# Kernel tuning notes

Measured on AMD Instinct MI355X. Metric: run time of the kernel, lower is better.

Reference implementation:

```python
import jax, jax.numpy as jnp
import numpy as np

B, T = 64, 20
VOCAB, E, CE, ANS = 20000, 300, 1024, 3000
H, N, W, R = 512, 256, 64, 4
RW = R * W
IF_SIZES = [RW, R, W, 1, W, W, R, 1, 1, 3 * R]  # read_keys, read_str, write_key, write_str, erase, write_vec, free, alloc_g, write_g, modes
IF_TOT = sum(IF_SIZES)
CLIP = 20.0
EPS = 1e-6


def _cosine_weights(mem, keys, strengths):
    # mem [B,N,W], keys [B,K,W], strengths [B,K] -> softmax over N
    mem_n = mem / (jnp.linalg.norm(mem, axis=-1, keepdims=True) + EPS)
    key_n = keys / (jnp.linalg.norm(keys, axis=-1, keepdims=True) + EPS)
    sim = jnp.einsum('bkw,bnw->bkn', key_n, mem_n)
    return jax.nn.softmax(sim * strengths[..., None], axis=-1)


def _init_state(b):
    z = lambda *s: jnp.zeros(s, jnp.float32)
    return (z(b, N, W), z(b, N, N), z(b, N), z(b, R, N), z(b, N), z(b, N), z(b, R, W), z(b, H), z(b, H))


def _dnc_step(Wih, Whh, b, Wif, bif, Wout, bout, state, x):
    mem, link, prec, wr, ww, usage, rvec, h, c = state
    bsz = x.shape[0]
    inp = jnp.concatenate([x, rvec.reshape(bsz, RW)], -1)
    gates = inp @ Wih + h @ Whh + b
    gi, gf, gg, go = jnp.split(gates, 4, -1)
    c = jax.nn.sigmoid(gf) * c + jax.nn.sigmoid(gi) * jnp.tanh(gg)
    h = jax.nn.sigmoid(go) * jnp.tanh(c)
    hc = jnp.clip(h, -CLIP, CLIP)
    xi = hc @ Wif + bif
    p = jnp.split(xi, np.cumsum(IF_SIZES)[:-1].tolist(), axis=-1)
    read_keys = jnp.tanh(p[0]).reshape(bsz, R, W)
    read_str = jax.nn.softplus(p[1])
    write_key = jnp.tanh(p[2]).reshape(bsz, 1, W)
    write_str = jax.nn.softplus(p[3])
    erase = jax.nn.sigmoid(p[4])
    write_vec = jnp.tanh(p[5])
    free = jax.nn.sigmoid(p[6])
    alloc_g = jax.nn.sigmoid(p[7])
    write_g = jax.nn.sigmoid(p[8])
    modes = jax.nn.softmax(p[9].reshape(bsz, R, 3), -1)

    # usage update and allocation (sort-based, data dependent)
    psi = jnp.prod(1.0 - free[..., None] * wr, axis=1)          # [B,N]
    usage = (usage + ww - usage * ww) * psi
    s_idx = jnp.argsort(usage, axis=-1)                          # ascending usage
    s_u = jnp.take_along_axis(usage, s_idx, -1)
    cp = jnp.cumprod(jnp.concatenate([jnp.ones_like(s_u[:, :1]), s_u[:, :-1]], -1), -1)
    a_sorted = (1.0 - s_u) * cp
    inv = jnp.argsort(s_idx, axis=-1)
    alloc = jnp.take_along_axis(a_sorted, inv, -1)

    # write
    cw = _cosine_weights(mem, write_key, write_str)[:, 0]        # [B,N]
    ww = write_g * (alloc_g * alloc + (1.0 - alloc_g) * cw)
    mem = mem * (1.0 - ww[..., None] * erase[:, None, :]) + ww[..., None] * write_vec[:, None, :]

    # temporal link matrix
    link = (1.0 - ww[:, :, None] - ww[:, None, :]) * link + ww[:, :, None] * prec[:, None, :]
    link = link * (1.0 - jnp.eye(N, dtype=link.dtype))
    prec = (1.0 - ww.sum(-1, keepdims=True)) * prec + ww

    # read
    fw = jnp.einsum('bij,brj->bri', link, wr)
    bw = jnp.einsum('bji,brj->bri', link, wr)
    cr = _cosine_weights(mem, read_keys, read_str)
    wr = modes[..., 0:1] * bw + modes[..., 1:2] * cr + modes[..., 2:3] * fw
    rvec = jnp.einsum('brn,bnw->brw', wr, mem)

    out = jnp.concatenate([hc, rvec.reshape(bsz, RW)], -1) @ Wout + bout
    out = jnp.clip(out, -CLIP, CLIP)
    return (mem, link, prec, wr, ww, usage, rvec, h, c), out


def _model(img_feat, emb, img_W, img_b, q_Wih, q_Whh, q_b, q_Wif, q_bif, q_Wout, q_bout,
           c_Wih, c_Whh, c_b, c_Wif, c_bif, c_Wout, c_bout, fc1_W, fc1_b, fc2_W, fc2_b, qst):
    bsz = qst.shape[0]
    # question encoder: embedding -> tanh -> DNC over time -> mean pool
    qv = jnp.tanh(emb[qst])                                      # [B,T,E]
    step = lambda st, x: _dnc_step(q_Wih, q_Whh, q_b, q_Wif, q_bif, q_Wout, q_bout, st, x)
    _, outs = jax.lax.scan(step, _init_state(bsz), jnp.swapaxes(qv, 0, 1))
    qfeat = outs.mean(0)                                         # [B,CE]
    # image encoder: fc on frozen VGG feature, L2 norm (norm detached)
    imgf = img_feat @ img_W + img_b
    imgf = imgf / jax.lax.stop_gradient(jnp.linalg.norm(imgf, axis=1, keepdims=True))
    comb = jnp.tanh(imgf * qfeat)
    # controller DNC: single timestep
    st_c, out_c = _dnc_step(c_Wih, c_Whh, c_b, c_Wif, c_bif, c_Wout, c_bout, _init_state(bsz), comb)
    rv_c = st_c[6].reshape(bsz, RW)
    last = jnp.tanh(jnp.concatenate([out_c, rv_c], -1))
    last = jnp.tanh(last @ fc1_W + fc1_b)
    return last @ fc2_W + fc2_b                                  # logits [B,ANS]


def setup_inputs():
    ks = jax.random.split(jax.random.key(0), 20)
    g = lambda k, s, sc=0.05: jax.random.normal(k, s, dtype=jnp.float32) * sc
    z = lambda *s: jnp.zeros(s, jnp.float32)
    return {
        'img_feat': g(ks[0], (B, 4096), 1.0),
        'qst': jax.random.randint(ks[1], (B, T), 0, VOCAB),
        'emb': g(ks[2], (VOCAB, E)),
        'img_W': g(ks[3], (4096, CE)), 'img_b': z(CE),
        'q_Wih': g(ks[4], (E + RW, 4 * H)), 'q_Whh': g(ks[5], (H, 4 * H)), 'q_b': z(4 * H),
        'q_Wif': g(ks[6], (H, IF_TOT)), 'q_bif': z(IF_TOT),
        'q_Wout': g(ks[7], (H + RW, CE)), 'q_bout': z(CE),
        'c_Wih': g(ks[8], (CE + RW, 4 * H)), 'c_Whh': g(ks[9], (H, 4 * H)), 'c_b': z(4 * H),
        'c_Wif': g(ks[10], (H, IF_TOT)), 'c_bif': z(IF_TOT),
        'c_Wout': g(ks[11], (H + RW, CE)), 'c_bout': z(CE),
        'fc1_W': g(ks[12], (CE + RW, ANS)), 'fc1_b': z(ANS),
        'fc2_W': g(ks[13], (ANS, ANS)), 'fc2_b': z(ANS),
    }


def reference(img_feat, qst, emb, img_W, img_b, q_Wih, q_Whh, q_b, q_Wif, q_bif, q_Wout, q_bout,
              c_Wih, c_Whh, c_b, c_Wif, c_bif, c_Wout, c_bout, fc1_W, fc1_b, fc2_W, fc2_b):
    return _model(img_feat, emb, img_W, img_b, q_Wih, q_Whh, q_b, q_Wif, q_bif, q_Wout, q_bout,
                  c_Wih, c_Whh, c_b, c_Wif, c_bif, c_Wout, c_bout, fc1_W, fc1_b, fc2_W, fc2_b, qst)
```

## Files before the change

### kernel.cpp

```cpp
#include <hip/hip_runtime.h>
#include <cmath>

#define CLIPV 20.0f
#define EPSV 1e-6f

__device__ __forceinline__ float sigmoidf_(float x){ return 1.0f/(1.0f + expf(-x)); }
__device__ __forceinline__ float softplusf_(float x){ return (x > 20.0f) ? x : log1pf(expf(x)); }
__device__ __forceinline__ float clipf_(float x){ return fminf(fmaxf(x, -CLIPV), CLIPV); }

__device__ __forceinline__ float wave_sum64(float v){
  #pragma unroll
  for (int off=32; off>=1; off>>=1) v += __shfl_xor(v, off, 64);
  return v;
}
__device__ __forceinline__ float wave_max64(float v){
  #pragma unroll
  for (int off=32; off>=1; off>>=1) v = fmaxf(v, __shfl_xor(v, off, 64));
  return v;
}
__device__ __forceinline__ float block_sum256(float v, float* s_red){
  v = wave_sum64(v);
  __syncthreads();
  if ((threadIdx.x & 63) == 0) s_red[threadIdx.x>>6] = v;
  __syncthreads();
  return s_red[0]+s_red[1]+s_red[2]+s_red[3];
}
__device__ __forceinline__ float block_max256(float v, float* s_red){
  v = wave_max64(v);
  __syncthreads();
  if ((threadIdx.x & 63) == 0) s_red[threadIdx.x>>6] = v;
  __syncthreads();
  return fmaxf(fmaxf(s_red[0],s_red[1]), fmaxf(s_red[2],s_red[3]));
}
template<int N>
__device__ __forceinline__ void block_sumN(float (&v)[N], float* scr){
  #pragma unroll
  for (int i=0;i<N;i++) v[i] = wave_sum64(v[i]);
  __syncthreads();
  if ((threadIdx.x & 63) == 0){
    int w = threadIdx.x >> 6;
    #pragma unroll
    for (int i=0;i<N;i++) scr[w*N + i] = v[i];
  }
  __syncthreads();
  #pragma unroll
  for (int i=0;i<N;i++) v[i] = scr[0*N+i] + scr[1*N+i] + scr[2*N+i] + scr[3*N+i];
}
template<int N>
__device__ __forceinline__ void block_maxN(float (&v)[N], float* scr){
  #pragma unroll
  for (int i=0;i<N;i++) v[i] = wave_max64(v[i]);
  __syncthreads();
  if ((threadIdx.x & 63) == 0){
    int w = threadIdx.x >> 6;
    #pragma unroll
    for (int i=0;i<N;i++) scr[w*N + i] = v[i];
  }
  __syncthreads();
  #pragma unroll
  for (int i=0;i<N;i++) v[i] = fmaxf(fmaxf(scr[0*N+i],scr[1*N+i]), fmaxf(scr[2*N+i],scr[3*N+i]));
}

__device__ __forceinline__ void cstore(float* p, float v){
  __hip_atomic_store(p, v, __ATOMIC_RELAXED, __HIP_MEMORY_SCOPE_AGENT);
}

#define WS_MEM    0
#define WS_LINK   1048576
#define WS_PREC   5242880
#define WS_WR     5275648
#define WS_WW     5341184
#define WS_USAGE  5357568
#define WS_BAR    5373952
#define WS_ZONEA  5374976
#define WS_QSUM   5374976
#define WS_HTS    5440512
#define WS_RVS    6128640
#define WS_XIS    6472704
#define WS_GXP    7105728
#define WS_ZONEC  9727168
#define WS_IMGF   10879168
#define WS_COMB   10944704
#define WS_LASTB  11010240
#define WS_HID1   11092160
#define WS_QV     11284160

__global__ void embed_kernel(const int* __restrict__ qst, const float* __restrict__ emb,
                             float* __restrict__ qv){
  int idx = blockIdx.x*256 + threadIdx.x;
  if (idx >= 1280*300) return;
  int m = idx / 300;
  int e = idx - m*300;
  int t = m >> 6, b = m & 63;
  int tok = qst[b*20 + t];
  qv[idx] = tanhf(emb[(size_t)tok*300 + e]);
}

__global__ __launch_bounds__(256) void gemm64(
    int M, int N, int Ktot, int KS,
    const float* __restrict__ A, int lda,
    const float* __restrict__ B,
    const float* __restrict__ bias,
    float* __restrict__ out, float* __restrict__ part, int mode)
{
  __shared__ float As[32*68];
  __shared__ float Bs[32*68];
  int tid = threadIdx.x;
  int nb = blockIdx.x*64, ks = blockIdx.y, mb = blockIdx.z*64;
  int Kc = (((Ktot + KS - 1)/KS) + 3) & ~3;
  int kbeg = ks*Kc, kend = min(Ktot, kbeg + Kc);
  int tm = tid >> 4, tn = tid & 15;
  float acc[4][4];
  #pragma unroll
  for (int i=0;i<4;i++){ acc[i][0]=0.f; acc[i][1]=0.f; acc[i][2]=0.f; acc[i][3]=0.f; }

  for (int k0 = kbeg; k0 < kend; k0 += 32){
    int klim = kend - k0; if (klim > 32) klim = 32;
    #pragma unroll
    for (int i=0;i<2;i++){
      int idx = tid + i*256;
      int m = idx >> 3, kq = (idx & 7) << 2;
      if (kq < klim){
        const float* ap = A + (size_t)(mb+m)*lda + k0 + kq;
        float4 v;
        if (kq + 3 < klim) v = *(const float4*)ap;
        else { v.x=ap[0]; v.y=(kq+1<klim)?ap[1]:0.f; v.z=(kq+2<klim)?ap[2]:0.f; v.w=0.f; }
        float* as = As + m;
        as[(kq+0)*68]=v.x; as[(kq+1)*68]=v.y; as[(kq+2)*68]=v.z; as[(kq+3)*68]=v.w;
      }
    }
    #pragma unroll
    for (int i=0;i<2;i++){
      int idx = tid + i*256;
      int kk = idx >> 4, nq = (idx & 15) << 2;
      int n = nb + nq;
      float4 v = {0.f,0.f,0.f,0.f};
      if (kk < klim && n < N){
        const float* bp = B + (size_t)(k0+kk)*N + n;
        if (n + 3 < N) v = *(const float4*)bp;
        else { v.x=bp[0]; v.y=(n+1<N)?bp[1]:0.f; v.z=(n+2<N)?bp[2]:0.f; }
      }
      *(float4*)(Bs + kk*68 + nq) = v;
    }
    __syncthreads();
    for (int kk = 0; kk < klim; kk++){
      float4 a = *(const float4*)(As + kk*68 + tm*4);
      float4 bv = *(const float4*)(Bs + kk*68 + tn*4);
      acc[0][0]+=a.x*bv.x; acc[0][1]+=a.x*bv.y; acc[0][2]+=a.x*bv.z; acc[0][3]+=a.x*bv.w;
      acc[1][0]+=a.y*bv.x; acc[1][1]+=a.y*bv.y; acc[1][2]+=a.y*bv.z; acc[1][3]+=a.y*bv.w;
      acc[2][0]+=a.z*bv.x; acc[2][1]+=a.z*bv.y; acc[2][2]+=a.z*bv.z; acc[2][3]+=a.z*bv.w;
      acc[3][0]+=a.w*bv.x; acc[3][1]+=a.w*bv.y; acc[3][2]+=a.w*bv.z; acc[3][3]+=a.w*bv.w;
    }
    __syncthreads();
  }

  #pragma unroll
  for (int i=0;i<4;i++){
    int m = tm*4 + i;
    #pragma unroll
    for (int j=0;j<4;j++){
      int n = nb + tn*4 + j;
      if (n < N){
        if (mode == 0){
          part[((size_t)(ks*64 + m))*N + n] = acc[i][j];
        } else {
          float v = acc[i][j] + (bias ? bias[n] : 0.f);
          if (mode == 2) v = tanhf(v);
          out[(size_t)(mb+m)*N + n] = v;
        }
      }
    }
  }
}

__global__ void reduce64(const float* __restrict__ part, int KS, int MN4, int N,
                         const float* __restrict__ bias, float* __restrict__ out, int mode){
  int idx = blockIdx.x*256 + threadIdx.x;
  if (idx >= MN4) return;
  int base = idx*4;
  int n = base % N;
  float4 s = {0.f,0.f,0.f,0.f};
  size_t stride = (size_t)MN4*4;
  for (int p=0;p<KS;p++){
    float4 t = *(const float4*)(part + (size_t)p*stride + base);
    s.x+=t.x; s.y+=t.y; s.z+=t.z; s.w+=t.w;
  }
  if (bias){
    float4 bb = *(const float4*)(bias + n);
    s.x+=bb.x; s.y+=bb.y; s.z+=bb.z; s.w+=bb.w;
  }
  if (mode == 1){ s.x=tanhf(s.x); s.y=tanhf(s.y); s.z=tanhf(s.z); s.w=tanhf(s.w); }
  *(float4*)(out + base) = s;
}

__global__ __launch_bounds__(256) void comb_kernel(const float* __restrict__ imgf,
                                                   const float* __restrict__ qsum,
                                                   float* __restrict__ comb){
  __shared__ float s_red[4];
  int b = blockIdx.x, tid = threadIdx.x;
  float ss = 0.f;
  for (int j = tid; j < 1024; j += 256){ float v = imgf[b*1024+j]; ss += v*v; }
  ss = wave_sum64(ss);
  if ((tid & 63) == 0) s_red[tid>>6] = ss;
  __syncthreads();
  float inv = 1.0f / sqrtf(s_red[0]+s_red[1]+s_red[2]+s_red[3]);
  for (int j = tid; j < 1024; j += 256)
    comb[b*1024+j] = tanhf(imgf[b*1024+j]*inv * qsum[b*1024+j]*0.05f);
}

__global__ void tanhrvec_kernel(const float* __restrict__ rvecT, float* __restrict__ lastB){
  int idx = blockIdx.x*256 + threadIdx.x;
  if (idx >= 16384) return;
  int b = idx & 63, i = idx >> 6;
  lastB[(size_t)b*1280 + 1024 + i] = tanhf(rvecT[i*64 + b]);
}

struct SD_t {
  float s_rk[256], s_rstr[4], s_wkey[64], s_erase[64], s_wvec[64];
  float s_free[4], s_modes[12], s_scal[3], s_pad0[1];
  float s_wr[1024];
  float s_wwnew[256], s_usage[256], s_prec[256], s_scan[256], s_sim[256];
  float s_C[1024], s_D[1024];
  float s_red[44], s_PQ[8];
};
struct SGLO_t { float red[4*768]; float g2[768]; };
struct Shm {
  float Wg[768*8];
  float Wo[768*4];
  float Wi[512*4];
  union { SGLO_t glo; SD_t d; } u;
};


__device__ __forceinline__ void gbar(int* subs, int* root, int* ggen, int epoch){
  __syncthreads();
  if (threadIdx.x == 0){
    asm volatile("s_waitcnt vmcnt(0)" ::: "memory");
    int g = blockIdx.x & 15;
    int old = __hip_atomic_fetch_add(&subs[g*16], 1, __ATOMIC_RELAXED, __HIP_MEMORY_SCOPE_AGENT);
    if (old == 16*epoch - 1){
      int r = __hip_atomic_fetch_add(root, 1, __ATOMIC_RELAXED, __HIP_MEMORY_SCOPE_AGENT);
      if (r == 16*epoch - 1){
        #pragma unroll
        for (int gg = 0; gg < 16; gg++)
          __hip_atomic_store(&ggen[gg*16], epoch, __ATOMIC_RELAXED, __HIP_MEMORY_SCOPE_AGENT);
      }
    }
    while (__hip_atomic_load(&ggen[g*16], __ATOMIC_RELAXED, __HIP_MEMORY_SCOPE_AGENT) < epoch)
      __builtin_amdgcn_s_sleep(2);
    asm volatile("" ::: "memory");
  }
  __syncthreads();
}

__global__ __launch_bounds__(256) void dnc_recur(
    int T, int outmode, int slot0,
    const float* __restrict__ xpart, const float* __restrict__ Wih_r,
    const float* __restrict__ Whh, const float* __restrict__ gb,
    const float* __restrict__ Wif, const float* __restrict__ bif,
    const float* __restrict__ Wout, const float* __restrict__ bout,
    float* __restrict__ ws, float* __restrict__ outbuf, int* __restrict__ barmem)
{
  __shared__ Shm sh;

  float* memS  = ws + WS_MEM;
  float* linkS = ws + WS_LINK;
  float* precB = ws + WS_PREC;
  float* wrS   = ws + WS_WR;
  float* wwS   = ws + WS_WW;
  float* usgS  = ws + WS_USAGE;
  float* htS   = ws + WS_HTS;
  float* rvS   = ws + WS_RVS;
  float* xiSl  = ws + WS_XIS;
  int* subs  = barmem;
  int* root  = barmem + 256;
  int* ggen  = barmem + 288;
  int* xict  = barmem + 576;
  int* subsH = barmem + 608;
  int* rootH = barmem + 896;

  int tid = threadIdx.x, bid = blockIdx.x;
  int lane = tid & 63, wid = tid >> 6;
  int b_ = tid & 63, q_ = tid >> 6;

  {
    int c2 = bid*2;
    float2* Wg2w = (float2*)sh.Wg;
    for (int e2 = tid; e2 < 3072; e2 += 256){
      int k = e2 >> 2, g = e2 & 3;
      const float* src = (k < 256) ? (Wih_r + (size_t)k*2048 + g*512 + c2)
                                   : (Whh + (size_t)(k-256)*2048 + g*512 + c2);
      Wg2w[e2] = *(const float2*)src;
    }
    int c4o = bid*4;
    float4* Wo4 = (float4*)sh.Wo;
    for (int k = tid; k < 768; k += 256)
      Wo4[k] = *(const float4*)(Wout + (size_t)k*1024 + c4o);
    if (bid < 118){
      for (int e = tid; e < 2048; e += 256){
        int k = e >> 2, c = e & 3;
        int col = c4o + c;
        sh.Wi[e] = (col < 471) ? Wif[(size_t)k*471 + col] : 0.f;
      }
    }
  }
  float bo = bout[bid*4 + q_];
  float bifv = 0.f;
  if (bid < 118 && bid*4 + q_ < 471) bifv = bif[bid*4 + q_];
  __syncthreads();

  float c_reg = 0.f;
  float qacc = 0.f;

  for (int t = 0; t < T; t++){
    int pp = t & 1, wp = (t + 1) & 1;

    {
      if (t > 0){
        float accG[8] = {0.f,0.f,0.f,0.f,0.f,0.f,0.f,0.f};
        float accO[4] = {0.f,0.f,0.f,0.f};
        const float* rvP = rvS + (size_t)(slot0+t-1)*16384;
        const float* hP  = htS + (size_t)(slot0+t-1)*32768;
        for (int c = 0; c < 12; c++){
          int k0 = c*64 + wid*16;
          bool isH = (k0 >= 256);
          const float* src = isH ? (hP + (size_t)(k0-256)*64) : (rvP + (size_t)k0*64);
          float a[16];
          #pragma unroll
          for (int u=0; u<16; u++) a[u] = src[u*64 + lane];
          #pragma unroll
          for (int u=0; u<16; u++){
            int k = k0 + u;
            float4 w0 = *(const float4*)(sh.Wg + (size_t)k*8);
            float4 w1 = *(const float4*)(sh.Wg + (size_t)k*8 + 4);
            int orow = isH ? (k - 256) : (512 + k);
            float4 wo = *(const float4*)(sh.Wo + (size_t)orow*4);
            float av = a[u];
            float ao = isH ? clipf_(av) : av;
            accG[0] += av*w0.x; accG[1] += av*w0.y; accG[2] += av*w0.z; accG[3] += av*w0.w;
            accG[4] += av*w1.x; accG[5] += av*w1.y; accG[6] += av*w1.z; accG[7] += av*w1.w;
            accO[0] += ao*wo.x; accO[1] += ao*wo.y; accO[2] += ao*wo.z; accO[3] += ao*wo.w;
          }
        }
        #pragma unroll
        for (int j=0;j<8;j++) sh.u.glo.red[wid*768 + j*64 + lane] = accG[j];
        #pragma unroll
        for (int j=0;j<4;j++) sh.u.glo.red[wid*768 + (8+j)*64 + lane] = accO[j];
      }
      __syncthreads();
      #pragma unroll
      for (int v=0; v<3; v++){
        int j = q_ + v*4;
        float s;
        if (j < 8){
          int col = (j>>1)*512 + bid*2 + (j&1);
          s = gb[col] + xpart[((size_t)(t*64 + b_))*2048 + col];
        } else {
          s = bo;
        }
        if (t > 0){
          s += sh.u.glo.red[0*768 + j*64 + b_];
          s += sh.u.glo.red[1*768 + j*64 + b_];
          s += sh.u.glo.red[2*768 + j*64 + b_];
          s += sh.u.glo.red[3*768 + j*64 + b_];
        }
        sh.u.glo.g2[j*64 + b_] = s;
      }
      __syncthreads();
      if (t > 0) qacc += clipf_(sh.u.glo.g2[(8+q_)*64 + b_]);
      if (tid < 128){
        int jj = q_;
        float gi = sh.u.glo.g2[(0+jj)*64 + b_];
        float gf = sh.u.glo.g2[(2+jj)*64 + b_];
        float gg = sh.u.glo.g2[(4+jj)*64 + b_];
        float go = sh.u.glo.g2[(6+jj)*64 + b_];
        float cn = sigmoidf_(gf)*c_reg + sigmoidf_(gi)*tanhf(gg);
        float hn = sigmoidf_(go)*tanhf(cn);
        c_reg = cn;
        int col = bid*2 + jj;
        cstore(&htS[(size_t)(slot0+t)*32768 + col*64 + b_], hn);
      }
    }

    __syncthreads();
    if (tid == 0){
      asm volatile("s_waitcnt vmcnt(0)" ::: "memory");
      int g = bid & 15;
      int old = __hip_atomic_fetch_add(&subsH[g*16], 1, __ATOMIC_RELAXED, __HIP_MEMORY_SCOPE_AGENT);
      if (old == 16*(t+1) - 1)
        __hip_atomic_fetch_add(rootH, 1, __ATOMIC_RELAXED, __HIP_MEMORY_SCOPE_AGENT);
    }

    if (bid < 118){
      if (tid == 0){
        while (__hip_atomic_load(rootH, __ATOMIC_RELAXED, __HIP_MEMORY_SCOPE_AGENT) < 16*(t+1))
          __builtin_amdgcn_s_sleep(1);
        asm volatile("" ::: "memory");
      }
      __syncthreads();
      float acc[4] = {0.f,0.f,0.f,0.f};
      const float* hP = htS + (size_t)(slot0+t)*32768;
      for (int c = 0; c < 8; c++){
        int k0 = c*64 + wid*16;
        float a[16];
        #pragma unroll
        for (int u=0; u<16; u++) a[u] = hP[(size_t)(k0+u)*64 + lane];
        #pragma unroll
        for (int u=0; u<16; u++){
          float4 wv = *(const float4*)(sh.Wi + (size_t)(k0+u)*4);
          float ac = clipf_(a[u]);
          acc[0] += ac*wv.x; acc[1] += ac*wv.y; acc[2] += ac*wv.z; acc[3] += ac*wv.w;
        }
      }
      #pragma unroll
      for (int j=0;j<4;j++) sh.u.glo.red[wid*256 + j*64 + lane] = acc[j];
      __syncthreads();
      {
        float s = bifv;
        #pragma unroll
        for (int w=0;w<4;w++) s += sh.u.glo.red[w*256 + q_*64 + b_];
        int col = bid*4 + q_;
        if (col < 471) cstore(&xiSl[(size_t)(slot0+t)*30144 + b_*471 + col], s);
      }
      __syncthreads();
      if (tid == 0)
        __hip_atomic_fetch_add(xict, 1, __ATOMIC_RELAXED, __HIP_MEMORY_SCOPE_AGENT);
    }

    if (bid < 64){
      SD_t& sd = sh.u.d;
      int b = bid;
      const float* prec_in  = precB + pp*16384;
      float*       prec_out = precB + wp*16384;

      for (int e = tid; e < 1024; e += 256){
        sd.s_wr[e] = wrS[(size_t)b*1024 + e];
        sd.s_C[e] = 0.f; sd.s_D[e] = 0.f;
      }
      float wwold = wwS[(size_t)b*256 + tid];
      sd.s_usage[tid] = usgS[(size_t)b*256 + tid];
      sd.s_prec[tid]  = prec_in[(size_t)b*256 + tid];

      if (tid == 0){
        while (__hip_atomic_load(xict, __ATOMIC_RELAXED, __HIP_MEMORY_SCOPE_AGENT) < 118*(t+1))
          __builtin_amdgcn_s_sleep(1);
        asm volatile("" ::: "memory");
      }
      __syncthreads();

      const float* xrow = xiSl + (size_t)(slot0+t)*30144 + (size_t)b*471;
      for (int idx = tid; idx < 471; idx += 256){
        float v = xrow[idx];
        if (idx < 256)       sd.s_rk[idx] = tanhf(v);
        else if (idx < 260)  sd.s_rstr[idx-256] = softplusf_(v);
        else if (idx < 324)  sd.s_wkey[idx-260] = v;
        else if (idx == 324) sd.s_scal[0] = softplusf_(v);
        else if (idx < 389)  sd.s_erase[idx-325] = sigmoidf_(v);
        else if (idx < 453)  sd.s_wvec[idx-389] = tanhf(v);
        else if (idx < 457)  sd.s_free[idx-453] = sigmoidf_(v);
        else if (idx == 457) sd.s_scal[1] = sigmoidf_(v);
        else if (idx == 458) sd.s_scal[2] = sigmoidf_(v);
        else                 sd.s_modes[idx-459] = v;
      }
      __syncthreads();

      if (tid < 4){
        float m0 = sd.s_modes[tid*3], m1 = sd.s_modes[tid*3+1], m2 = sd.s_modes[tid*3+2];
        float mx = fmaxf(m0, fmaxf(m1,m2));
        float e0 = expf(m0-mx), e1 = expf(m1-mx), e2 = expf(m2-mx);
        float s = e0+e1+e2;
        sd.s_modes[tid*3] = e0/s; sd.s_modes[tid*3+1] = e1/s; sd.s_modes[tid*3+2] = e2/s;
      }
      {
        float k = sd.s_rk[wid*64 + lane];
        float ss = wave_sum64(k*k);
        sd.s_rk[wid*64 + lane] = k / (sqrtf(ss) + EPSV);
      }
      if (wid == 0){
        float k = sd.s_wkey[lane];
        float ss = wave_sum64(k*k);
        sd.s_wkey[lane] = k / (sqrtf(ss) + EPSV);
      }

      {
        float psi = 1.f;
        #pragma unroll
        for (int r=0;r<4;r++) psi *= (1.f - sd.s_free[r]*sd.s_wr[r*256+tid]);
        float u = (sd.s_usage[tid] + wwold - sd.s_usage[tid]*wwold) * psi;
        sd.s_usage[tid] = u;
        usgS[(size_t)b*256 + tid] = u;
      }
      __syncthreads();

      int rank_r;
      {
        float u = sd.s_usage[tid];
        int rank = 0;
        #pragma unroll 4
        for (int j4=0;j4<256;j4+=4){
          float4 uv = *(const float4*)(sd.s_usage + j4);
          rank += (uv.x < u) || (uv.x == u && (j4+0) < tid);
          rank += (uv.y < u) || (uv.y == u && (j4+1) < tid);
          rank += (uv.z < u) || (uv.z == u && (j4+2) < tid);
          rank += (uv.w < u) || (uv.w == u && (j4+3) < tid);
        }
        rank_r = rank;
        sd.s_scan[rank] = u;
      }
      __syncthreads();

      {
        float v = sd.s_scan[tid];
        #pragma unroll
        for (int off=1; off<64; off<<=1){
          float u2 = __shfl_up(v, off, 64);
          if (lane >= off) v *= u2;
        }
        if (lane == 63) sd.s_red[wid] = v;
        __syncthreads();
        float pre = 1.f;
        if (wid > 0) pre *= sd.s_red[0];
        if (wid > 1) pre *= sd.s_red[1];
        if (wid > 2) pre *= sd.s_red[2];
        v *= pre;
        sd.s_scan[tid] = v;
        __syncthreads();
      }
      float alloc_r;
      {
        float u = sd.s_usage[tid];
        float cpe = (rank_r > 0) ? sd.s_scan[rank_r-1] : 1.f;
        alloc_r = (1.f - u) * cpe;
      }

      {
        const float4* Mrow = (const float4*)(memS + (size_t)b*16384 + (size_t)tid*64);
        float nrm2 = 0.f, dt = 0.f;
        #pragma unroll
        for (int c4 = 0; c4 < 16; c4++){
          float4 mv = Mrow[c4];
          int w0 = c4*4;
          nrm2 += mv.x*mv.x + mv.y*mv.y + mv.z*mv.z + mv.w*mv.w;
          dt += mv.x*sd.s_wkey[w0] + mv.y*sd.s_wkey[w0+1] + mv.z*sd.s_wkey[w0+2] + mv.w*sd.s_wkey[w0+3];
        }
        sd.s_sim[tid] = dt / (sqrtf(nrm2)+EPSV) * sd.s_scal[0];
      }
      __syncthreads();

      {
        float v = sd.s_sim[tid];
        float mx = block_max256(v, sd.s_red);
        float e = expf(v - mx);
        float sm = block_sum256(e, sd.s_red);
        float cw = e / sm;
        float wwn = sd.s_scal[2] * (sd.s_scal[1]*alloc_r + (1.f - sd.s_scal[1])*cw);
        sd.s_wwnew[tid] = wwn;
        wwS[(size_t)b*256 + tid] = wwn;
        float r9[9];
        r9[0] = wwn;
        #pragma unroll
        for (int r=0;r<4;r++) r9[1+r] = sd.s_prec[tid]*sd.s_wr[r*256+tid];
        #pragma unroll
        for (int r=0;r<4;r++) r9[5+r] = wwn*sd.s_wr[r*256+tid];
        block_sumN<9>(r9, sd.s_red + 4);
        prec_out[(size_t)b*256 + tid] = (1.f - r9[0])*sd.s_prec[tid] + wwn;
        if (tid == 0){
          #pragma unroll
          for (int r=0;r<4;r++){ sd.s_PQ[r] = r9[1+r]; sd.s_PQ[4+r] = r9[5+r]; }
        }
      }
      __syncthreads();

      float aA[4] = {0,0,0,0}, aB[4] = {0,0,0,0};
      {
        const float4* Lrow = (const float4*)(linkS + (size_t)b*65536 + (size_t)tid*256);
        for (int c4 = 0; c4 < 64; c4++){
          float4 lv = Lrow[c4];
          int j = c4*4;
          float w0n = sd.s_wwnew[j], w1n = sd.s_wwnew[j+1], w2n = sd.s_wwnew[j+2], w3n = sd.s_wwnew[j+3];
          #pragma unroll
          for (int r=0;r<4;r++){
            float wr0 = sd.s_wr[r*256+j], wr1 = sd.s_wr[r*256+j+1];
            float wr2 = sd.s_wr[r*256+j+2], wr3 = sd.s_wr[r*256+j+3];
            aA[r] += lv.x*wr0 + lv.y*wr1 + lv.z*wr2 + lv.w*wr3;
            aB[r] += lv.x*(w0n*wr0) + lv.y*(w1n*wr1) + lv.z*(w2n*wr2) + lv.w*(w3n*wr3);
          }
        }
      }
      __syncthreads();

      {
        int cg = tid & 63, ioff = tid >> 6;
        int j0 = cg*4;
        float wwj0 = sd.s_wwnew[j0], wwj1 = sd.s_wwnew[j0+1], wwj2 = sd.s_wwnew[j0+2], wwj3 = sd.s_wwnew[j0+3];
        float pj0 = sd.s_prec[j0], pj1 = sd.s_prec[j0+1], pj2 = sd.s_prec[j0+2], pj3 = sd.s_prec[j0+3];
        float cC[4][4] = {{0}}, cD[4][4] = {{0}};
        float4* Lb = (float4*)(linkS + (size_t)b*65536);
        for (int it = 0; it < 64; it++){
          int i = it*4 + ioff;
          float4 lv = Lb[(size_t)i*64 + cg];
          float wwi = sd.s_wwnew[i];
          float4 ln;
          ln.x = (1.f - wwi - wwj0)*lv.x + wwi*pj0;
          ln.y = (1.f - wwi - wwj1)*lv.y + wwi*pj1;
          ln.z = (1.f - wwi - wwj2)*lv.z + wwi*pj2;
          ln.w = (1.f - wwi - wwj3)*lv.w + wwi*pj3;
          if (i >= j0 && i < j0+4){
            if (i == j0)        ln.x = 0.f;
            else if (i == j0+1) ln.y = 0.f;
            else if (i == j0+2) ln.z = 0.f;
            else                ln.w = 0.f;
          }
          Lb[(size_t)i*64 + cg] = ln;
          #pragma unroll
          for (int r=0;r<4;r++){
            float wri = sd.s_wr[r*256+i];
            float vbi = wwi*wri;
            cC[r][0] += lv.x*wri; cC[r][1] += lv.y*wri; cC[r][2] += lv.z*wri; cC[r][3] += lv.w*wri;
            cD[r][0] += lv.x*vbi; cD[r][1] += lv.y*vbi; cD[r][2] += lv.z*vbi; cD[r][3] += lv.w*vbi;
          }
        }
        for (int w=0; w<4; w++){
          if (ioff == w){
            #pragma unroll
            for (int r=0;r<4;r++){
              sd.s_C[r*256+j0+0] += cC[r][0]; sd.s_C[r*256+j0+1] += cC[r][1];
              sd.s_C[r*256+j0+2] += cC[r][2]; sd.s_C[r*256+j0+3] += cC[r][3];
              sd.s_D[r*256+j0+0] += cD[r][0]; sd.s_D[r*256+j0+1] += cD[r][1];
              sd.s_D[r*256+j0+2] += cD[r][2]; sd.s_D[r*256+j0+3] += cD[r][3];
            }
          }
          __syncthreads();
        }
      }

      float pr[4];
      {
        float4* Mrow = (float4*)(memS + (size_t)b*16384 + (size_t)tid*64);
        float wwn = sd.s_wwnew[tid];
        float nrm2 = 0.f, d0=0.f, d1=0.f, d2=0.f, d3=0.f;
        #pragma unroll
        for (int c4 = 0; c4 < 16; c4++){
          float4 mv = Mrow[c4];
          int w0 = c4*4;
          mv.x = mv.x*(1.f - wwn*sd.s_erase[w0+0]) + wwn*sd.s_wvec[w0+0];
          mv.y = mv.y*(1.f - wwn*sd.s_erase[w0+1]) + wwn*sd.s_wvec[w0+1];
          mv.z = mv.z*(1.f - wwn*sd.s_erase[w0+2]) + wwn*sd.s_wvec[w0+2];
          mv.w = mv.w*(1.f - wwn*sd.s_erase[w0+3]) + wwn*sd.s_wvec[w0+3];
          Mrow[c4] = mv;
          nrm2 += mv.x*mv.x + mv.y*mv.y + mv.z*mv.z + mv.w*mv.w;
          d0 += mv.x*sd.s_rk[w0] + mv.y*sd.s_rk[w0+1] + mv.z*sd.s_rk[w0+2] + mv.w*sd.s_rk[w0+3];
          d1 += mv.x*sd.s_rk[64+w0] + mv.y*sd.s_rk[64+w0+1] + mv.z*sd.s_rk[64+w0+2] + mv.w*sd.s_rk[64+w0+3];
          d2 += mv.x*sd.s_rk[128+w0] + mv.y*sd.s_rk[128+w0+1] + mv.z*sd.s_rk[128+w0+2] + mv.w*sd.s_rk[128+w0+3];
          d3 += mv.x*sd.s_rk[192+w0] + mv.y*sd.s_rk[192+w0+1] + mv.z*sd.s_rk[192+w0+2] + mv.w*sd.s_rk[192+w0+3];
        }
        float inv = 1.f/(sqrtf(nrm2)+EPSV);
        pr[0] = d0*inv*sd.s_rstr[0];
        pr[1] = d1*inv*sd.s_rstr[1];
        pr[2] = d2*inv*sd.s_rstr[2];
        pr[3] = d3*inv*sd.s_rstr[3];
      }
      {
        float m4[4] = {pr[0], pr[1], pr[2], pr[3]};
        block_maxN<4>(m4, sd.s_red + 4);
        float e4[4];
        #pragma unroll
        for (int r=0;r<4;r++) e4[r] = expf(pr[r] - m4[r]);
        float s4[4] = {e4[0], e4[1], e4[2], e4[3]};
        block_sumN<4>(s4, sd.s_red + 4);
        #pragma unroll
        for (int r=0;r<4;r++) pr[r] = e4[r]/s4[r];
      }
      __syncthreads();

      {
        float wwn = sd.s_wwnew[tid], pn = sd.s_prec[tid];
        #pragma unroll
        for (int r=0;r<4;r++){
          float wro = sd.s_wr[r*256+tid];
          float fw  = (1.f-wwn)*aA[r] - aB[r] + wwn*(sd.s_PQ[r] - pn*wro);
          float bwv = (1.f-wwn)*sd.s_C[r*256+tid] - sd.s_D[r*256+tid] + pn*(sd.s_PQ[4+r] - wwn*wro);
          float wrn = sd.s_modes[r*3+0]*bwv + sd.s_modes[r*3+1]*pr[r] + sd.s_modes[r*3+2]*fw;
          wrS[(size_t)b*1024 + r*256 + tid] = wrn;
          sd.s_wr[r*256+tid] = wrn;
        }
      }
      __syncthreads();

      {
        int r = tid >> 6, w = tid & 63;
        const float* Mb = memS + (size_t)b*16384;
        float acc = 0.f;
        for (int n=0; n<256; n++) acc += sd.s_wr[r*256+n]*Mb[(size_t)n*64 + w];
        cstore(&rvS[(size_t)(slot0+t)*16384 + (r*64 + w)*64 + b], acc);
      }
    }

    gbar(subs, root, ggen, t+1);
  }

  {
    float accO[4] = {0.f,0.f,0.f,0.f};
    const float* rvP = rvS + (size_t)(slot0+T-1)*16384;
    const float* hP  = htS + (size_t)(slot0+T-1)*32768;
    for (int c = 0; c < 12; c++){
      int k0 = c*64 + wid*16;
      bool isH = (k0 >= 256);
      const float* src = isH ? (hP + (size_t)(k0-256)*64) : (rvP + (size_t)k0*64);
      float a[16];
      #pragma unroll
      for (int u=0; u<16; u++) a[u] = src[u*64 + lane];
      #pragma unroll
      for (int u=0; u<16; u++){
        int k = k0 + u;
        int orow = isH ? (k - 256) : (512 + k);
        float4 wo = *(const float4*)(sh.Wo + (size_t)orow*4);
        float av = isH ? clipf_(a[u]) : a[u];
        accO[0] += av*wo.x; accO[1] += av*wo.y; accO[2] += av*wo.z; accO[3] += av*wo.w;
      }
    }
    #pragma unroll
    for (int j=0;j<4;j++) sh.u.glo.red[wid*256 + j*64 + lane] = accO[j];
    __syncthreads();
    float v = bo;
    #pragma unroll
    for (int w=0;w<4;w++) v += sh.u.glo.red[w*256 + q_*64 + b_];
    v = clipf_(v);
    if (outmode == 0){
      qacc += v;
      outbuf[(size_t)b_*1024 + (bid*4 + q_)] = qacc;
    } else {
      outbuf[(size_t)b_*1280 + (bid*4 + q_)] = tanhf(v);
    }
  }
}

extern "C" void kernel_launch(void* const* d_in, const int* in_sizes, int n_in,
                              void* d_out, int out_size, void* d_ws, size_t ws_size,
                              hipStream_t stream) {
  const float* img_feat = (const float*)d_in[0];
  const int*   qst      = (const int*)  d_in[1];
  const float* emb      = (const float*)d_in[2];
  const float* img_W    = (const float*)d_in[3];
  const float* img_b    = (const float*)d_in[4];
  const float* q_Wih    = (const float*)d_in[5];
  const float* q_Whh    = (const float*)d_in[6];
  const float* q_b      = (const float*)d_in[7];
  const float* q_Wif    = (const float*)d_in[8];
  const float* q_bif    = (const float*)d_in[9];
  const float* q_Wout   = (const float*)d_in[10];
  const float* q_bout   = (const float*)d_in[11];
  const float* c_Wih    = (const float*)d_in[12];
  const float* c_Whh    = (const float*)d_in[13];
  const float* c_b      = (const float*)d_in[14];
  const float* c_Wif    = (const float*)d_in[15];
  const float* c_bif    = (const float*)d_in[16];
  const float* c_Wout   = (const float*)d_in[17];
  const float* c_bout   = (const float*)d_in[18];
  const float* fc1_W    = (const float*)d_in[19];
  const float* fc1_b    = (const float*)d_in[20];
  const float* fc2_W    = (const float*)d_in[21];
  const float* fc2_b    = (const float*)d_in[22];

  float* ws = (float*)d_ws;
  float* qv    = ws + WS_QV;
  float* gxp   = ws + WS_GXP;
  float* zoneC = ws + WS_ZONEC;
  float* imgf  = ws + WS_IMGF;
  float* combB = ws + WS_COMB;
  float* lastB = ws + WS_LASTB;
  float* hid1  = ws + WS_HID1;
  float* qsum  = ws + WS_QSUM;
  int*   bar   = (int*)(ws + WS_BAR);

  hipMemsetAsync(ws, 0, (size_t)WS_ZONEA*4, stream);

  embed_kernel<<<1500, 256, 0, stream>>>(qst, emb, qv);

  gemm64<<<dim3(16,16,1), 256, 0, stream>>>(64, 1024, 4096, 16,
      img_feat, 4096, img_W, nullptr, nullptr, zoneC, 0);
  reduce64<<<64, 256, 0, stream>>>(zoneC, 16, 16384, 1024, img_b, imgf, 0);

  gemm64<<<dim3(32,1,20), 256, 0, stream>>>(1280, 2048, 300, 1,
      qv, 300, q_Wih, nullptr, gxp, nullptr, 1);

  dnc_recur<<<256, 256, 0, stream>>>(20, 0, 0,
      gxp, q_Wih + (size_t)300*2048, q_Whh, q_b,
      q_Wif, q_bif, q_Wout, q_bout, ws, qsum, bar);

  comb_kernel<<<64, 256, 0, stream>>>(imgf, qsum, combB);

  hipMemsetAsync(ws, 0, (size_t)WS_ZONEA*4, stream);

  gemm64<<<dim3(32,4,1), 256, 0, stream>>>(64, 2048, 1024, 4,
      combB, 1024, c_Wih, nullptr, nullptr, zoneC, 0);
  reduce64<<<128, 256, 0, stream>>>(zoneC, 4, 32768, 2048, nullptr, gxp, 0);

  dnc_recur<<<256, 256, 0, stream>>>(1, 1, 20,
      gxp, c_Wih + (size_t)1024*2048, c_Whh, c_b,
      c_Wif, c_bif, c_Wout, c_bout, ws, lastB, bar);

  tanhrvec_kernel<<<64, 256, 0, stream>>>(ws + WS_RVS + (size_t)20*16384, lastB);

  gemm64<<<dim3(47,5,1), 256, 0, stream>>>(64, 3000, 1280, 5,
      lastB, 1280, fc1_W, nullptr, nullptr, zoneC, 0);
  reduce64<<<188, 256, 0, stream>>>(zoneC, 5, 48000, 3000, fc1_b, hid1, 1);

  gemm64<<<dim3(47,6,1), 256, 0, stream>>>(64, 3000, 3000, 6,
      hid1, 3000, fc2_W, nullptr, nullptr, zoneC, 0);
  reduce64<<<188, 256, 0, stream>>>(zoneC, 6, 48000, 3000, fc2_b, (float*)d_out, 0);
}
```

Before: 2.100 ms.

## Move output projection off the LSTM critical path and reassign interface blocks

The per-step output projection (Wout accumulation) is split out of the gate GEMV into a separate routine. Blocks that do not compute interface vectors now run it while waiting for the interface/memory stage, and interface blocks run it after publishing xi. The interface-vector work moves from blocks 0-117 to blocks 138 and up, so it no longer shares blocks with the 64 memory-update blocks. The aim is to shorten the serial h->xi->memory chain per timestep. The cost is reading the activations twice per step and extra syncthreads.

```diff
diff --git a/kernel.cpp b/kernel.cpp
--- a/kernel.cpp
+++ b/kernel.cpp
@@ -215,6 +215,8 @@
   lastB[(size_t)b*1280 + 1024 + i] = tanhf(rvecT[i*64 + b]);
 }
 
+#define I_LO 138
+
 struct SD_t {
   float s_rk[256], s_rstr[4], s_wkey[64], s_erase[64], s_wvec[64];
   float s_free[4], s_modes[12], s_scal[3], s_pad0[1];
@@ -231,6 +233,38 @@
   union { SGLO_t glo; SD_t d; } u;
 };
 
+__device__ __forceinline__ float glo_opart(const float* __restrict__ rvP,
+                                           const float* __restrict__ hP,
+                                           const float* __restrict__ WoL,
+                                           float* __restrict__ red,
+                                           float bo, int lane, int wid, int b_, int q_){
+  float accO[4] = {0.f,0.f,0.f,0.f};
+  for (int c = 0; c < 12; c++){
+    int k0 = c*64 + wid*16;
+    bool isH = (k0 >= 256);
+    const float* src = isH ? (hP + (size_t)(k0-256)*64) : (rvP + (size_t)k0*64);
+    float a[16];
+    #pragma unroll
+    for (int u=0; u<16; u++) a[u] = src[u*64 + lane];
+    #pragma unroll
+    for (int u=0; u<16; u++){
+      int k = k0 + u;
+      int orow = isH ? (k - 256) : (512 + k);
+      float4 wo = *(const float4*)(WoL + (size_t)orow*4);
+      float av = isH ? clipf_(a[u]) : a[u];
+      accO[0] += av*wo.x; accO[1] += av*wo.y; accO[2] += av*wo.z; accO[3] += av*wo.w;
+    }
+  }
+  #pragma unroll
+  for (int j=0;j<4;j++) red[wid*256 + j*64 + lane] = accO[j];
+  __syncthreads();
+  float v = bo;
+  #pragma unroll
+  for (int w=0;w<4;w++) v += red[w*256 + q_*64 + b_];
+  __syncthreads();
+  return v;
+}
+
 
 __device__ __forceinline__ void gbar(int* subs, int* root, int* ggen, int epoch){
   __syncthreads();
@@ -282,6 +316,7 @@
   int tid = threadIdx.x, bid = blockIdx.x;
   int lane = tid & 63, wid = tid >> 6;
   int b_ = tid & 63, q_ = tid >> 6;
+  bool isI = (bid >= I_LO);
 
   {
     int c2 = bid*2;
@@ -296,17 +331,18 @@
     float4* Wo4 = (float4*)sh.Wo;
     for (int k = tid; k < 768; k += 256)
       Wo4[k] = *(const float4*)(Wout + (size_t)k*1024 + c4o);
-    if (bid < 118){
+    if (isI){
+      int c4i = (bid - I_LO)*4;
       for (int e = tid; e < 2048; e += 256){
         int k = e >> 2, c = e & 3;
-        int col = c4o + c;
+        int col = c4i + c;
         sh.Wi[e] = (col < 471) ? Wif[(size_t)k*471 + col] : 0.f;
       }
     }
   }
   float bo = bout[bid*4 + q_];
   float bifv = 0.f;
-  if (bid < 118 && bid*4 + q_ < 471) bifv = bif[bid*4 + q_];
+  if (isI && (bid - I_LO)*4 + q_ < 471) bifv = bif[(bid - I_LO)*4 + q_];
   __syncthreads();
 
   float c_reg = 0.f;
@@ -314,17 +350,16 @@
 
   for (int t = 0; t < T; t++){
     int pp = t & 1, wp = (t + 1) & 1;
+    const float* rvP1 = rvS + (size_t)(slot0+t-1)*16384;
+    const float* hP1  = htS + (size_t)(slot0+t-1)*32768;
 
     {
       if (t > 0){
         float accG[8] = {0.f,0.f,0.f,0.f,0.f,0.f,0.f,0.f};
-        float accO[4] = {0.f,0.f,0.f,0.f};
-        const float* rvP = rvS + (size_t)(slot0+t-1)*16384;
-        const float* hP  = htS + (size_t)(slot0+t-1)*32768;
         for (int c = 0; c < 12; c++){
           int k0 = c*64 + wid*16;
           bool isH = (k0 >= 256);
-          const float* src = isH ? (hP + (size_t)(k0-256)*64) : (rvP + (size_t)k0*64);
+          const float* src = isH ? (hP1 + (size_t)(k0-256)*64) : (rvP1 + (size_t)k0*64);
           float a[16];
           #pragma unroll
           for (int u=0; u<16; u++) a[u] = src[u*64 + lane];
@@ -333,31 +368,20 @@
             int k = k0 + u;
             float4 w0 = *(const float4*)(sh.Wg + (size_t)k*8);
             float4 w1 = *(const float4*)(sh.Wg + (size_t)k*8 + 4);
-            int orow = isH ? (k - 256) : (512 + k);
-            float4 wo = *(const float4*)(sh.Wo + (size_t)orow*4);
             float av = a[u];
-            float ao = isH ? clipf_(av) : av;
             accG[0] += av*w0.x; accG[1] += av*w0.y; accG[2] += av*w0.z; accG[3] += av*w0.w;
             accG[4] += av*w1.x; accG[5] += av*w1.y; accG[6] += av*w1.z; accG[7] += av*w1.w;
-            accO[0] += ao*wo.x; accO[1] += ao*wo.y; accO[2] += ao*wo.z; accO[3] += ao*wo.w;
           }
         }
         #pragma unroll
         for (int j=0;j<8;j++) sh.u.glo.red[wid*768 + j*64 + lane] = accG[j];
-        #pragma unroll
-        for (int j=0;j<4;j++) sh.u.glo.red[wid*768 + (8+j)*64 + lane] = accO[j];
       }
       __syncthreads();
       #pragma unroll
-      for (int v=0; v<3; v++){
+      for (int v=0; v<2; v++){
         int j = q_ + v*4;
-        float s;
-        if (j < 8){
-          int col = (j>>1)*512 + bid*2 + (j&1);
-          s = gb[col] + xpart[((size_t)(t*64 + b_))*2048 + col];
-        } else {
-          s = bo;
-        }
+        int col = (j>>1)*512 + bid*2 + (j&1);
+        float s = gb[col] + xpart[((size_t)(t*64 + b_))*2048 + col];
         if (t > 0){
           s += sh.u.glo.red[0*768 + j*64 + b_];
           s += sh.u.glo.red[1*768 + j*64 + b_];
@@ -367,7 +391,6 @@
         sh.u.glo.g2[j*64 + b_] = s;
       }
       __syncthreads();
-      if (t > 0) qacc += clipf_(sh.u.glo.g2[(8+q_)*64 + b_]);
       if (tid < 128){
         int jj = q_;
         float gi = sh.u.glo.g2[(0+jj)*64 + b_];
@@ -391,7 +414,12 @@
         __hip_atomic_fetch_add(rootH, 1, __ATOMIC_RELAXED, __HIP_MEMORY_SCOPE_AGENT);
     }
 
-    if (bid < 118){
+    if (!isI && t > 0){
+      float v = glo_opart(rvP1, hP1, sh.Wo, sh.u.glo.red, bo, lane, wid, b_, q_);
+      qacc += clipf_(v);
+    }
+
+    if (isI){
       if (tid == 0){
         while (__hip_atomic_load(rootH, __ATOMIC_RELAXED, __HIP_MEMORY_SCOPE_AGENT) < 16*(t+1))
           __builtin_amdgcn_s_sleep(1);
@@ -419,12 +447,16 @@
         float s = bifv;
         #pragma unroll
         for (int w=0;w<4;w++) s += sh.u.glo.red[w*256 + q_*64 + b_];
-        int col = bid*4 + q_;
+        int col = (bid - I_LO)*4 + q_;
         if (col < 471) cstore(&xiSl[(size_t)(slot0+t)*30144 + b_*471 + col], s);
       }
       __syncthreads();
       if (tid == 0)
         __hip_atomic_fetch_add(xict, 1, __ATOMIC_RELAXED, __HIP_MEMORY_SCOPE_AGENT);
+      if (t > 0){
+        float v = glo_opart(rvP1, hP1, sh.Wo, sh.u.glo.red, bo, lane, wid, b_, q_);
+        qacc += clipf_(v);
+      }
     }
 
     if (bid < 64){
@@ -700,31 +732,9 @@
   }
 
   {
-    float accO[4] = {0.f,0.f,0.f,0.f};
-    const float* rvP = rvS + (size_t)(slot0+T-1)*16384;
-    const float* hP  = htS + (size_t)(slot0+T-1)*32768;
-    for (int c = 0; c < 12; c++){
-      int k0 = c*64 + wid*16;
-      bool isH = (k0 >= 256);
-      const float* src = isH ? (hP + (size_t)(k0-256)*64) : (rvP + (size_t)k0*64);
-      float a[16];
-      #pragma unroll
-      for (int u=0; u<16; u++) a[u] = src[u*64 + lane];
-      #pragma unroll
-      for (int u=0; u<16; u++){
-        int k = k0 + u;
-        int orow = isH ? (k - 256) : (512 + k);
-        float4 wo = *(const float4*)(sh.Wo + (size_t)orow*4);
-        float av = isH ? clipf_(a[u]) : a[u];
-        accO[0] += av*wo.x; accO[1] += av*wo.y; accO[2] += av*wo.z; accO[3] += av*wo.w;
-      }
-    }
-    #pragma unroll
-    for (int j=0;j<4;j++) sh.u.glo.red[wid*256 + j*64 + lane] = accO[j];
-    __syncthreads();
-    float v = bo;
-    #pragma unroll
-    for (int w=0;w<4;w++) v += sh.u.glo.red[w*256 + q_*64 + b_];
+    float v = glo_opart(rvS + (size_t)(slot0+T-1)*16384,
+                        htS + (size_t)(slot0+T-1)*32768,
+                        sh.Wo, sh.u.glo.red, bo, lane, wid, b_, q_);
     v = clipf_(v);
     if (outmode == 0){
       qacc += v;
```

Result: no change. 2.066 ms (median of 3 runs) (-1.6%).
